# Kernel tuning notes

Hardware: AMD Instinct MI355X
Metric: run time of the kernel (lower is better)

## Reference

```python
import jax, jax.numpy as jnp
import numpy as np

B, T, DIM, HEADS, DH = 4, 2048, 1024, 16, 64
MAX_SEQ_LEN = 2048


def setup_inputs() -> dict:
    key = jax.random.key(0)
    k1, k2, k3, k4 = jax.random.split(key, 4)
    x = jax.random.normal(k1, (B, T, DIM), dtype=jnp.float32)
    W_qkv = jax.random.normal(k2, (DIM, 3 * HEADS * DH), dtype=jnp.float32) * (DIM ** -0.5)
    W_0 = jax.random.normal(k3, (HEADS * DH, DIM), dtype=jnp.float32) * ((HEADS * DH) ** -0.5)
    rel_bias = jax.random.normal(k4, (2 * MAX_SEQ_LEN - 1, HEADS), dtype=jnp.float32) * 0.02
    return {"x": x, "W_qkv": W_qkv, "W_0": W_0, "rel_bias": rel_bias}


def reference(x, W_qkv, W_0, rel_bias):
    b, t, dim = x.shape
    heads = rel_bias.shape[1]
    dh = W_qkv.shape[1] // (3 * heads)
    scale = dh ** -0.5

    qkv = x @ W_qkv  # (b, t, 3*heads*dh), feature layout is (d, k, h): d slowest, h fastest
    qkv = qkv.reshape(b, t, dh, 3, heads)
    qkv = jnp.transpose(qkv, (3, 0, 4, 1, 2))  # (3, b, h, t, d)
    q, k, v = qkv[0], qkv[1], qkv[2]

    scores = jnp.einsum('bhid,bhjd->bhij', q, k) * scale  # (b, h, t, t)

    causal = jnp.tril(jnp.ones((t, t), dtype=bool))
    scores = jnp.where(causal[None, None], scores, -jnp.inf)

    # relative position bias: index = j - i + t - 1
    rel_idx = jnp.arange(t)[None, :] - jnp.arange(t)[:, None] + (t - 1)  # (t, t)
    bias = rel_bias[rel_idx]  # (t, t, heads)
    scores = scores + jnp.transpose(bias, (2, 0, 1))[None]

    attn = jax.nn.softmax(scores, axis=-1)
    out = jnp.einsum('bhij,bhjd->bhid', attn, v)  # (b, h, t, d)
    out = jnp.transpose(out, (0, 2, 1, 3)).reshape(b, t, heads * dh)
    return out @ W_0
```

## Files before the change

kernel.cpp:

```cpp
#include <hip/hip_runtime.h>
#include <hip/hip_bf16.h>
#include <stdint.h>

#define B_ 4
#define T_ 2048
#define NH 16
#define DH 64
#define DIM 1024
#define NF 3072
#define QKS 2048

typedef unsigned short u16;
typedef uint32_t u32;
typedef __bf16 bf16;
typedef bf16 bf16x8 __attribute__((ext_vector_type(8)));
typedef float f32x4 __attribute__((ext_vector_type(4)));
typedef u16 u16x8 __attribute__((ext_vector_type(8)));
typedef u16 u16x4 __attribute__((ext_vector_type(4)));

__device__ __forceinline__ u16 f2bf(float f) {
    u32 u = __builtin_bit_cast(u32, f);
    u = (u + 0x7fffu + ((u >> 16) & 1u)) >> 16;
    return (u16)u;
}

__device__ __forceinline__ float exp2f_fast(float x) {
#if __has_builtin(__builtin_amdgcn_exp2f)
    return __builtin_amdgcn_exp2f(x);
#else
    return exp2f(x);
#endif
}

#define GLOAD16(g, l)                                                          \
    __builtin_amdgcn_global_load_lds(                                          \
        (const __attribute__((address_space(1))) u32*)(g),                     \
        (__attribute__((address_space(3))) u32*)(l), 16, 0, 0)


__global__ __launch_bounds__(256) void cvt_bf16_k(const float* __restrict__ src,
                                                  u16* __restrict__ dst, int n8) {
    int i = blockIdx.x * 256 + threadIdx.x;
    if (i >= n8) return;
    const float4* s = (const float4*)src + (size_t)i * 2;
    float4 a = s[0], b = s[1];
    u16x8 o;
    o[0]=f2bf(a.x); o[1]=f2bf(a.y); o[2]=f2bf(a.z); o[3]=f2bf(a.w);
    o[4]=f2bf(b.x); o[5]=f2bf(b.y); o[6]=f2bf(b.z); o[7]=f2bf(b.w);
    *(u16x8*)(dst + (size_t)i * 8) = o;
}

template <int PERM>
__global__ __launch_bounds__(256) void wcvt_t_k(const float* __restrict__ src,
                                                u16* __restrict__ dst, int K, int N) {
    __shared__ float tile[32][33];
    int n0 = blockIdx.x * 32, k0 = blockIdx.y * 32;
    int c = threadIdx.x & 31, r0 = threadIdx.x >> 5;
#pragma unroll
    for (int i = 0; i < 4; i++) {
        int r = r0 + i * 8;
        tile[r][c] = src[(size_t)(k0 + r) * N + n0 + c];
    }
    __syncthreads();
#pragma unroll
    for (int i = 0; i < 4; i++) {
        int r = r0 + i * 8;
        int n = n0 + r;
        int nd;
        if (PERM) {
            int d = n / 48, rem = n - d * 48;
            int kk = rem >> 4, h = rem & 15;
            nd = kk * 1024 + h * 64 + d;
        } else {
            nd = n;
        }
        dst[(size_t)nd * K + k0 + c] = f2bf(tile[c][r]);
    }
}

__global__ __launch_bounds__(256) void rbt_k(const float* __restrict__ rb,
                                             u16* __restrict__ rbT2,
                                             u16* __restrict__ rbT2s) {
    int i = blockIdx.x * 256 + threadIdx.x;
    if (i >= NH * 4096) return;
    int h = i >> 12, d = i & 4095;
    float v = (d <= 2047) ? rb[(size_t)d * NH + h] * 1.44269504f : -1e30f;
    rbT2[i] = __builtin_bit_cast(u16, (bf16)v);
    int d2 = d + 1;
    float v2 = (d2 <= 2047) ? rb[(size_t)d2 * NH + h] * 1.44269504f : -1e30f;
    rbT2s[i] = __builtin_bit_cast(u16, (bf16)v2);
}


template <int OUTMODE>
__global__ __launch_bounds__(256, 2) void gemm_bt_k(const u16* __restrict__ A,
                                                    const u16* __restrict__ Bt,
                                                    void* __restrict__ Cout,
                                                    int M, int N, int K) {
    __shared__ __align__(16) u16 As[128 * 64];
    __shared__ __align__(16) u16 Bs[128 * 64];
    const int tid = threadIdx.x;
    const int wave = tid >> 6, lane = tid & 63;
    const int bm = blockIdx.x, bn = blockIdx.y;
    const int wr = (wave >> 1) * 64, wc = (wave & 1) * 64;
    const int lrow = lane & 15, g4 = lane >> 4;
    const int srow8 = lane >> 3;
    const int scs = (lane & 7) ^ srow8;
    const u16* Ab = A + (size_t)(bm * 128 + wave * 32) * K;
    const u16* Bb = Bt + (size_t)(bn * 128 + wave * 32) * K;
    u16* AsW = As + wave * 2048;
    u16* BsW = Bs + wave * 2048;
    f32x4 acc[4][4] = {};

    for (int k0 = 0; k0 < K; k0 += 64) {
        __syncthreads();
#pragma unroll
        for (int g = 0; g < 4; g++) {
            GLOAD16(Ab + (size_t)(g * 8 + srow8) * K + k0 + scs * 8, AsW + g * 512);
            GLOAD16(Bb + (size_t)(g * 8 + srow8) * K + k0 + scs * 8, BsW + g * 512);
        }
        __syncthreads();
#pragma unroll
        for (int kk2 = 0; kk2 < 2; kk2++) {
            bf16x8 af[4], bfr[4];
#pragma unroll
            for (int i = 0; i < 4; i++)
                af[i] = *(const bf16x8*)&As[(wr + i * 16 + lrow) * 64 +
                                            (((kk2 * 4 + g4) ^ (lrow & 7)) * 8)];
#pragma unroll
            for (int j = 0; j < 4; j++)
                bfr[j] = *(const bf16x8*)&Bs[(wc + j * 16 + lrow) * 64 +
                                             (((kk2 * 4 + g4) ^ (lrow & 7)) * 8)];
#pragma unroll
            for (int i = 0; i < 4; i++)
#pragma unroll
                for (int j = 0; j < 4; j++) {
                    if (OUTMODE == 2)
                        acc[i][j] = __builtin_amdgcn_mfma_f32_16x16x32_bf16(
                            bfr[j], af[i], acc[i][j], 0, 0, 0);
                    else
                        acc[i][j] = __builtin_amdgcn_mfma_f32_16x16x32_bf16(
                            af[i], bfr[j], acc[i][j], 0, 0, 0);
                }
        }
    }

    const int crow = (lane >> 4) * 4, ccol = lane & 15;
    if (OUTMODE == 2) {
        u16* Vt = (u16*)Cout;
#pragma unroll
        for (int i = 0; i < 4; i++)
#pragma unroll
            for (int j = 0; j < 4; j++) {
                int gm = bm * 128 + wr + i * 16 + ccol;
                int b = gm >> 11, tt = gm & 2047;
#pragma unroll
                for (int r = 0; r < 4; r++) {
                    int f = bn * 128 + wc + j * 16 + crow + r;
                    int h = f >> 6, d = f & 63;
                    Vt[(((size_t)(b * NH + h)) * DH + d) * T_ + tt] =
                        f2bf(acc[i][j][r]);
                }
            }
    } else {
#pragma unroll
        for (int i = 0; i < 4; i++)
#pragma unroll
            for (int j = 0; j < 4; j++) {
                int gm = bm * 128 + wr + i * 16 + crow;
                int gn = bn * 128 + wc + j * 16 + ccol;
#pragma unroll
                for (int r = 0; r < 4; r++) {
                    if (OUTMODE == 1)
                        ((u16*)Cout)[(size_t)(gm + r) * N + gn] = f2bf(acc[i][j][r]);
                    else
                        ((float*)Cout)[(size_t)(gm + r) * N + gn] = acc[i][j][r];
                }
            }
    }
}

__global__ __launch_bounds__(256, 2) void flash_attn_k(const u16* __restrict__ qkF,
                                                       const u16* __restrict__ Vt,
                                                       const u16* __restrict__ rbT2,
                                                       const u16* __restrict__ rbT2s,
                                                       u16* __restrict__ O) {
    __shared__ __align__(16) u16 Ks[64 * 64];
    __shared__ __align__(16) u16 Vs[64 * 64];
    __shared__ __align__(16) u16 Ps[4][2][16 * 64];
    __shared__ __align__(16) u16 rbs2a[4096];
    __shared__ __align__(16) u16 rbs2b[4096];
    const int tid = threadIdx.x, wave = tid >> 6, lane = tid & 63;
    const int Lid = blockIdx.x;
    const int c = Lid & 7, u = Lid >> 3;
    const int bh = ((u & 7) << 3) | c;
    const int pair = u >> 3;
    const int h = bh & 15, b = bh >> 4;
    const int l15 = lane & 15, g4 = lane >> 4;
    const float SC2 = 0.125f * 1.44269504f;

    {
        *(u16x8*)&rbs2a[tid * 8] = *(const u16x8*)&rbT2[(size_t)h * 4096 + tid * 8];
        *(u16x8*)&rbs2a[2048 + tid * 8] = *(const u16x8*)&rbT2[(size_t)h * 4096 + 2048 + tid * 8];
        *(u16x8*)&rbs2b[tid * 8] = *(const u16x8*)&rbT2s[(size_t)h * 4096 + tid * 8];
        *(u16x8*)&rbs2b[2048 + tid * 8] = *(const u16x8*)&rbT2s[(size_t)h * 4096 + 2048 + tid * 8];
    }

    const size_t trow = (size_t)b * T_;
    const int srow = tid >> 2;
    const int sch = tid & 3;
    u16* pwA = &Ps[wave][0][0];
    u16* pwB = &Ps[wave][1][0];
    const u16* kgb = &qkF[(trow + srow) * QKS + 1024 + h * 64];
    const u16* vgb = &Vt[((size_t)bh * DH + srow) * T_];

    u16x8 kv0 = *(const u16x8*)&kgb[sch * 8];
    u16x8 kv1 = *(const u16x8*)&kgb[(sch + 4) * 8];
    u16x8 vv0 = *(const u16x8*)&vgb[sch * 8];
    u16x8 vv1 = *(const u16x8*)&vgb[(sch + 4) * 8];

    for (int half = 0; half < 2; half++) {
        const int blk = half ? 15 - pair : pair;
        const int qbA = blk * 128 + wave * 16;
        const int qbB = qbA + 64;
        bf16x8 aqA[2], aqB[2];
        aqA[0] = *(const bf16x8*)&qkF[(trow + qbA + l15) * QKS + h * 64 + g4 * 8];
        aqA[1] = *(const bf16x8*)&qkF[(trow + qbA + l15) * QKS + h * 64 + 32 + g4 * 8];
        aqB[0] = *(const bf16x8*)&qkF[(trow + qbB + l15) * QKS + h * 64 + g4 * 8];
        aqB[1] = *(const bf16x8*)&qkF[(trow + qbB + l15) * QKS + h * 64 + 32 + g4 * 8];

        const int ibA = 2047 - l15 + g4 * 4 - qbA;
        const u32* b32A = (const u32*)((ibA & 1) ? &rbs2b[ibA - 1] : &rbs2a[ibA]);
        const u32* b32B = b32A - 32;

        f32x4 oaccA[4] = {}, oaccB[4] = {};
        float lA = 0.f, lB = 0.f;

        const int jtmax = 2 * blk + 1;
        for (int jt = 0; jt <= jtmax; jt++) {
            const int j0 = jt * 64;
            __syncthreads();
            {
                int sw = srow & 7;
                *(u16x8*)&Ks[srow * 64 + ((sch ^ sw) * 8)] = kv0;
                *(u16x8*)&Ks[srow * 64 + (((sch + 4) ^ sw) * 8)] = kv1;
                *(u16x8*)&Vs[srow * 64 + ((sch ^ sw) * 8)] = vv0;
                *(u16x8*)&Vs[srow * 64 + (((sch + 4) ^ sw) * 8)] = vv1;
            }
            __syncthreads();
            {
                int njt = jt + 1;
                int j0n = (njt <= jtmax) ? njt * 64 : (half == 0 ? 0 : -1);
                if (j0n >= 0) {
                    const u16* kg = kgb + (size_t)j0n * QKS;
                    const u16* vg = vgb + j0n;
                    kv0 = *(const u16x8*)&kg[sch * 8];
                    kv1 = *(const u16x8*)&kg[(sch + 4) * 8];
                    vv0 = *(const u16x8*)&vg[sch * 8];
                    vv1 = *(const u16x8*)&vg[(sch + 4) * 8];
                }
            }
            f32x4 sA[4], sB[4];
#pragma unroll
            for (int ni = 0; ni < 4; ni++) {
                f32x4 z = {};
                sA[ni] = z;
                sB[ni] = z;
            }
            __builtin_amdgcn_s_setprio(1);
#pragma unroll
            for (int ni = 0; ni < 4; ni++) {
                int arow = ni * 16 + l15;
#pragma unroll
                for (int kk = 0; kk < 2; kk++) {
                    int ch = kk * 4 + g4;
                    bf16x8 ak = *(const bf16x8*)&Ks[arow * 64 + ((ch ^ (arow & 7)) * 8)];
                    sA[ni] = __builtin_amdgcn_mfma_f32_16x16x32_bf16(ak, aqA[kk], sA[ni], 0, 0, 0);
                    sB[ni] = __builtin_amdgcn_mfma_f32_16x16x32_bf16(ak, aqB[kk], sB[ni], 0, 0, 0);
                }
            }
            __builtin_amdgcn_s_setprio(0);
            const int jo = j0 >> 1;
            {
                float su = 0.f;
#pragma unroll
                for (int ni = 0; ni < 4; ni++) {
                    u32 w0 = b32A[jo + ni * 8];
                    u32 w1 = b32A[jo + ni * 8 + 1];
                    float e0 = exp2f_fast(fmaf(sA[ni][0], SC2, __builtin_bit_cast(float, w0 << 16)));
                    float e1 = exp2f_fast(fmaf(sA[ni][1], SC2, __builtin_bit_cast(float, w0 & 0xffff0000u)));
                    float e2 = exp2f_fast(fmaf(sA[ni][2], SC2, __builtin_bit_cast(float, w1 << 16)));
                    float e3 = exp2f_fast(fmaf(sA[ni][3], SC2, __builtin_bit_cast(float, w1 & 0xffff0000u)));
                    su += (e0 + e1) + (e2 + e3);
                    u16x4 pk;
                    pk[0] = __builtin_bit_cast(u16, (bf16)e0);
                    pk[1] = __builtin_bit_cast(u16, (bf16)e1);
                    pk[2] = __builtin_bit_cast(u16, (bf16)e2);
                    pk[3] = __builtin_bit_cast(u16, (bf16)e3);
                    int colb = ni * 16 + g4 * 4;
                    int ch = colb >> 3, co = colb & 7;
                    *(u16x4*)&pwA[l15 * 64 + ((ch ^ (l15 & 7)) * 8) + co] = pk;
                }
                su += __shfl_xor(su, 16);
                su += __shfl_xor(su, 32);
                lA += su;
            }
            {
                float su = 0.f;
#pragma unroll
                for (int ni = 0; ni < 4; ni++) {
                    u32 w0 = b32B[jo + ni * 8];
                    u32 w1 = b32B[jo + ni * 8 + 1];
                    float e0 = exp2f_fast(fmaf(sB[ni][0], SC2, __builtin_bit_cast(float, w0 << 16)));
                    float e1 = exp2f_fast(fmaf(sB[ni][1], SC2, __builtin_bit_cast(float, w0 & 0xffff0000u)));
                    float e2 = exp2f_fast(fmaf(sB[ni][2], SC2, __builtin_bit_cast(float, w1 << 16)));
                    float e3 = exp2f_fast(fmaf(sB[ni][3], SC2, __builtin_bit_cast(float, w1 & 0xffff0000u)));
                    su += (e0 + e1) + (e2 + e3);
                    u16x4 pk;
                    pk[0] = __builtin_bit_cast(u16, (bf16)e0);
                    pk[1] = __builtin_bit_cast(u16, (bf16)e1);
                    pk[2] = __builtin_bit_cast(u16, (bf16)e2);
                    pk[3] = __builtin_bit_cast(u16, (bf16)e3);
                    int colb = ni * 16 + g4 * 4;
                    int ch = colb >> 3, co = colb & 7;
                    *(u16x4*)&pwB[l15 * 64 + ((ch ^ (l15 & 7)) * 8) + co] = pk;
                }
                su += __shfl_xor(su, 16);
                su += __shfl_xor(su, 32);
                lB += su;
            }
            bf16x8 bpA[2], bpB[2];
#pragma unroll
            for (int kk = 0; kk < 2; kk++) {
                int ch = kk * 4 + g4;
                int off = l15 * 64 + ((ch ^ (l15 & 7)) * 8);
                bpA[kk] = *(const bf16x8*)&pwA[off];
                bpB[kk] = *(const bf16x8*)&pwB[off];
            }
            __builtin_amdgcn_s_setprio(1);
#pragma unroll
            for (int di = 0; di < 4; di++) {
                int vrow = di * 16 + l15;
#pragma unroll
                for (int kk = 0; kk < 2; kk++) {
                    int ch = kk * 4 + g4;
                    bf16x8 av = *(const bf16x8*)&Vs[vrow * 64 + ((ch ^ (vrow & 7)) * 8)];
                    oaccA[di] = __builtin_amdgcn_mfma_f32_16x16x32_bf16(av, bpA[kk], oaccA[di], 0, 0, 0);
                    oaccB[di] = __builtin_amdgcn_mfma_f32_16x16x32_bf16(av, bpB[kk], oaccB[di], 0, 0, 0);
                }
            }
            __builtin_amdgcn_s_setprio(0);
        }
        {
            float inv = 1.0f / lA;
            u16* orow = &O[((size_t)b * T_ + qbA + l15) * (NH * DH) + h * DH];
#pragma unroll
            for (int di = 0; di < 4; di++) {
                u16x4 ov;
#pragma unroll
                for (int r = 0; r < 4; r++)
                    ov[r] = __builtin_bit_cast(u16, (bf16)(oaccA[di][r] * inv));
                *(u16x4*)&orow[di * 16 + g4 * 4] = ov;
            }
        }
        {
            float inv = 1.0f / lB;
            u16* orow = &O[((size_t)b * T_ + qbB + l15) * (NH * DH) + h * DH];
#pragma unroll
            for (int di = 0; di < 4; di++) {
                u16x4 ov;
#pragma unroll
                for (int r = 0; r < 4; r++)
                    ov[r] = __builtin_bit_cast(u16, (bf16)(oaccB[di][r] * inv));
                *(u16x4*)&orow[di * 16 + g4 * 4] = ov;
            }
        }
    }
}


extern "C" void kernel_launch(void* const* d_in, const int* in_sizes, int n_in,
                              void* d_out, int out_size, void* d_ws, size_t ws_size,
                              hipStream_t stream) {
    const float* x    = (const float*)d_in[0];
    const float* Wqkv = (const float*)d_in[1];
    const float* W0   = (const float*)d_in[2];
    const float* rb   = (const float*)d_in[3];
    char* ws = (char*)d_ws;

    u16*   xb    = (u16*)(ws + 0);
    u16*   WqkvT = (u16*)(ws + 16777216);
    u16*   W0T   = (u16*)(ws + 23068672);
    u16*   rbT2  = (u16*)(ws + 25165824);
    u16*   rbT2s = (u16*)(ws + 25296896);
    u16*   qkF   = (u16*)(ws + 25427968);
    u16*   attnO = (u16*)(ws + 58982400);
    u16*   Vtb   = (u16*)(ws + 75759616);

    cvt_bf16_k<<<4096, 256, 0, stream>>>(x, xb, (B_ * T_ * DIM) / 8);
    wcvt_t_k<1><<<dim3(NF / 32, DIM / 32), 256, 0, stream>>>(Wqkv, WqkvT, DIM, NF);
    wcvt_t_k<0><<<dim3(DIM / 32, DIM / 32), 256, 0, stream>>>(W0, W0T, DIM, DIM);
    rbt_k<<<(NH * 4096 + 255) / 256, 256, 0, stream>>>(rb, rbT2, rbT2s);

    gemm_bt_k<1><<<dim3((B_ * T_) / 128, QKS / 128), 256, 0, stream>>>(
        xb, WqkvT, qkF, B_ * T_, QKS, DIM);

    gemm_bt_k<2><<<dim3((B_ * T_) / 128, (NF - QKS) / 128), 256, 0, stream>>>(
        xb, WqkvT + (size_t)QKS * DIM, Vtb, B_ * T_, NF - QKS, DIM);

    flash_attn_k<<<512, 256, 0, stream>>>(qkF, Vtb, rbT2, rbT2s, attnO);

    gemm_bt_k<0><<<dim3((B_ * T_) / 128, DIM / 128), 256, 0, stream>>>(
        attnO, W0T, d_out, B_ * T_, DIM, DIM);
}
```

Measured before the change: 177.9 us.

## Double-buffer K/V tiles in flash attention and merge QK and V projection GEMMs

The attention kernel now keeps two LDS buffers for K and V. The next tile is written to the alternate buffer after the PV MFMAs, so each iteration needs one barrier instead of two. Separately, the Q/K and V projection GEMMs are fused into one launch over all 3072 output columns, with blocks where bn>=16 writing the transposed V layout. This removes a kernel launch and tail. In exchange the attention kernel uses 16KB more LDS, which could lower occupancy at 2 blocks per CU, and the GEMM has a runtime branch around its MFMA loop.

```diff
diff --git a/kernel.cpp b/kernel.cpp
--- a/kernel.cpp
+++ b/kernel.cpp
@@ -96,6 +96,7 @@
 __global__ __launch_bounds__(256, 2) void gemm_bt_k(const u16* __restrict__ A,
                                                     const u16* __restrict__ Bt,
                                                     void* __restrict__ Cout,
+                                                    u16* __restrict__ Vt,
                                                     int M, int N, int K) {
     __shared__ __align__(16) u16 As[128 * 64];
     __shared__ __align__(16) u16 Bs[128 * 64];
@@ -110,6 +111,7 @@
     const u16* Bb = Bt + (size_t)(bn * 128 + wave * 32) * K;
     u16* AsW = As + wave * 2048;
     u16* BsW = Bs + wave * 2048;
+    const bool vt = (OUTMODE == 1) && (bn >= 16);
     f32x4 acc[4][4] = {};
 
     for (int k0 = 0; k0 < K; k0 += 64) {
@@ -131,23 +133,26 @@
             for (int j = 0; j < 4; j++)
                 bfr[j] = *(const bf16x8*)&Bs[(wc + j * 16 + lrow) * 64 +
                                              (((kk2 * 4 + g4) ^ (lrow & 7)) * 8)];
-#pragma unroll
-            for (int i = 0; i < 4; i++)
-#pragma unroll
-                for (int j = 0; j < 4; j++) {
-                    if (OUTMODE == 2)
+            if (vt) {
+#pragma unroll
+                for (int i = 0; i < 4; i++)
+#pragma unroll
+                    for (int j = 0; j < 4; j++)
                         acc[i][j] = __builtin_amdgcn_mfma_f32_16x16x32_bf16(
                             bfr[j], af[i], acc[i][j], 0, 0, 0);
-                    else
+            } else {
+#pragma unroll
+                for (int i = 0; i < 4; i++)
+#pragma unroll
+                    for (int j = 0; j < 4; j++)
                         acc[i][j] = __builtin_amdgcn_mfma_f32_16x16x32_bf16(
                             af[i], bfr[j], acc[i][j], 0, 0, 0);
-                }
+            }
         }
     }
 
     const int crow = (lane >> 4) * 4, ccol = lane & 15;
-    if (OUTMODE == 2) {
-        u16* Vt = (u16*)Cout;
+    if (vt) {
 #pragma unroll
         for (int i = 0; i < 4; i++)
 #pragma unroll
@@ -156,7 +161,7 @@
                 int b = gm >> 11, tt = gm & 2047;
 #pragma unroll
                 for (int r = 0; r < 4; r++) {
-                    int f = bn * 128 + wc + j * 16 + crow + r;
+                    int f = (bn - 16) * 128 + wc + j * 16 + crow + r;
                     int h = f >> 6, d = f & 63;
                     Vt[(((size_t)(b * NH + h)) * DH + d) * T_ + tt] =
                         f2bf(acc[i][j][r]);
@@ -185,8 +190,8 @@
                                                        const u16* __restrict__ rbT2,
                                                        const u16* __restrict__ rbT2s,
                                                        u16* __restrict__ O) {
-    __shared__ __align__(16) u16 Ks[64 * 64];
-    __shared__ __align__(16) u16 Vs[64 * 64];
+    __shared__ __align__(16) u16 Ks[2][64 * 64];
+    __shared__ __align__(16) u16 Vs[2][64 * 64];
     __shared__ __align__(16) u16 Ps[4][2][16 * 64];
     __shared__ __align__(16) u16 rbs2a[4096];
     __shared__ __align__(16) u16 rbs2b[4096];
@@ -209,6 +214,7 @@
     const size_t trow = (size_t)b * T_;
     const int srow = tid >> 2;
     const int sch = tid & 3;
+    const int sw = srow & 7;
     u16* pwA = &Ps[wave][0][0];
     u16* pwB = &Ps[wave][1][0];
     const u16* kgb = &qkF[(trow + srow) * QKS + 1024 + h * 64];
@@ -218,6 +224,12 @@
     u16x8 kv1 = *(const u16x8*)&kgb[(sch + 4) * 8];
     u16x8 vv0 = *(const u16x8*)&vgb[sch * 8];
     u16x8 vv1 = *(const u16x8*)&vgb[(sch + 4) * 8];
+    *(u16x8*)&Ks[0][srow * 64 + ((sch ^ sw) * 8)] = kv0;
+    *(u16x8*)&Ks[0][srow * 64 + (((sch + 4) ^ sw) * 8)] = kv1;
+    *(u16x8*)&Vs[0][srow * 64 + ((sch ^ sw) * 8)] = vv0;
+    *(u16x8*)&Vs[0][srow * 64 + (((sch + 4) ^ sw) * 8)] = vv1;
+    __syncthreads();
+    int cur = 0;
 
     for (int half = 0; half < 2; half++) {
         const int blk = half ? 15 - pair : pair;
@@ -239,27 +251,17 @@
         const int jtmax = 2 * blk + 1;
         for (int jt = 0; jt <= jtmax; jt++) {
             const int j0 = jt * 64;
-            __syncthreads();
-            {
-                int sw = srow & 7;
-                *(u16x8*)&Ks[srow * 64 + ((sch ^ sw) * 8)] = kv0;
-                *(u16x8*)&Ks[srow * 64 + (((sch + 4) ^ sw) * 8)] = kv1;
-                *(u16x8*)&Vs[srow * 64 + ((sch ^ sw) * 8)] = vv0;
-                *(u16x8*)&Vs[srow * 64 + (((sch + 4) ^ sw) * 8)] = vv1;
-            }
-            __syncthreads();
-            {
-                int njt = jt + 1;
-                int j0n = (njt <= jtmax) ? njt * 64 : (half == 0 ? 0 : -1);
-                if (j0n >= 0) {
-                    const u16* kg = kgb + (size_t)j0n * QKS;
-                    const u16* vg = vgb + j0n;
-                    kv0 = *(const u16x8*)&kg[sch * 8];
-                    kv1 = *(const u16x8*)&kg[(sch + 4) * 8];
-                    vv0 = *(const u16x8*)&vg[sch * 8];
-                    vv1 = *(const u16x8*)&vg[(sch + 4) * 8];
-                }
-            }
+            const int j0n = (jt + 1 <= jtmax) ? (jt + 1) * 64 : (half == 0 ? 0 : -1);
+            if (j0n >= 0) {
+                const u16* kg = kgb + (size_t)j0n * QKS;
+                const u16* vg = vgb + j0n;
+                kv0 = *(const u16x8*)&kg[sch * 8];
+                kv1 = *(const u16x8*)&kg[(sch + 4) * 8];
+                vv0 = *(const u16x8*)&vg[sch * 8];
+                vv1 = *(const u16x8*)&vg[(sch + 4) * 8];
+            }
+            const u16* KsC = &Ks[cur][0];
+            const u16* VsC = &Vs[cur][0];
             f32x4 sA[4], sB[4];
 #pragma unroll
             for (int ni = 0; ni < 4; ni++) {
@@ -274,7 +276,7 @@
 #pragma unroll
                 for (int kk = 0; kk < 2; kk++) {
                     int ch = kk * 4 + g4;
-                    bf16x8 ak = *(const bf16x8*)&Ks[arow * 64 + ((ch ^ (arow & 7)) * 8)];
+                    bf16x8 ak = *(const bf16x8*)&KsC[arow * 64 + ((ch ^ (arow & 7)) * 8)];
                     sA[ni] = __builtin_amdgcn_mfma_f32_16x16x32_bf16(ak, aqA[kk], sA[ni], 0, 0, 0);
                     sB[ni] = __builtin_amdgcn_mfma_f32_16x16x32_bf16(ak, aqB[kk], sB[ni], 0, 0, 0);
                 }
@@ -344,12 +346,22 @@
 #pragma unroll
                 for (int kk = 0; kk < 2; kk++) {
                     int ch = kk * 4 + g4;
-                    bf16x8 av = *(const bf16x8*)&Vs[vrow * 64 + ((ch ^ (vrow & 7)) * 8)];
+                    bf16x8 av = *(const bf16x8*)&VsC[vrow * 64 + ((ch ^ (vrow & 7)) * 8)];
                     oaccA[di] = __builtin_amdgcn_mfma_f32_16x16x32_bf16(av, bpA[kk], oaccA[di], 0, 0, 0);
                     oaccB[di] = __builtin_amdgcn_mfma_f32_16x16x32_bf16(av, bpB[kk], oaccB[di], 0, 0, 0);
                 }
             }
             __builtin_amdgcn_s_setprio(0);
+            if (j0n >= 0) {
+                u16* Kn = &Ks[cur ^ 1][0];
+                u16* Vn = &Vs[cur ^ 1][0];
+                *(u16x8*)&Kn[srow * 64 + ((sch ^ sw) * 8)] = kv0;
+                *(u16x8*)&Kn[srow * 64 + (((sch + 4) ^ sw) * 8)] = kv1;
+                *(u16x8*)&Vn[srow * 64 + ((sch ^ sw) * 8)] = vv0;
+                *(u16x8*)&Vn[srow * 64 + (((sch + 4) ^ sw) * 8)] = vv1;
+            }
+            __syncthreads();
+            cur ^= 1;
         }
         {
             float inv = 1.0f / lA;
@@ -402,14 +414,11 @@
     wcvt_t_k<0><<<dim3(DIM / 32, DIM / 32), 256, 0, stream>>>(W0, W0T, DIM, DIM);
     rbt_k<<<(NH * 4096 + 255) / 256, 256, 0, stream>>>(rb, rbT2, rbT2s);
 
-    gemm_bt_k<1><<<dim3((B_ * T_) / 128, QKS / 128), 256, 0, stream>>>(
-        xb, WqkvT, qkF, B_ * T_, QKS, DIM);
-
-    gemm_bt_k<2><<<dim3((B_ * T_) / 128, (NF - QKS) / 128), 256, 0, stream>>>(
-        xb, WqkvT + (size_t)QKS * DIM, Vtb, B_ * T_, NF - QKS, DIM);
+    gemm_bt_k<1><<<dim3((B_ * T_) / 128, NF / 128), 256, 0, stream>>>(
+        xb, WqkvT, qkF, Vtb, B_ * T_, QKS, DIM);
 
     flash_attn_k<<<512, 256, 0, stream>>>(qkF, Vtb, rbT2, rbT2s, attnO);
 
     gemm_bt_k<0><<<dim3((B_ * T_) / 128, DIM / 128), 256, 0, stream>>>(
-        attnO, W0T, d_out, B_ * T_, DIM, DIM);
-}
+        attnO, W0T, d_out, nullptr, B_ * T_, DIM, DIM);
+}
```

After: 167.2 us. 1.06x faster.
